# Performance work log

Hardware: AMD Instinct MI355X
Metric: run time of the kernel (lower is better)

## Reference

```python
import jax, jax.numpy as jnp
import numpy as np

GLYPH_DIM = 4096
PADDING_IDX = GLYPH_DIM  # 4096
GLYPH_EMB = 20           # CHAR_EMB 16 + COLOR_EMB 4
HIDDEN = 32
MAX_LEN = 64


def setup_inputs() -> dict:
    key = jax.random.key(0)
    k1, k2, k3, k4, k5, k6, k7 = jax.random.split(key, 7)
    B, H, W = 8192, 21, 79
    glyph_chars = jax.random.randint(k1, (B, H, W), 0, 256, dtype=jnp.int32)
    glyph_colors = jax.random.randint(k2, (B, H, W), 0, 16, dtype=jnp.int32)
    # Embedding table with zero padding row (torch padding_idx semantics)
    emb_table = jax.random.normal(k3, (GLYPH_DIM + 1, GLYPH_EMB), dtype=jnp.float32) * 0.02
    emb_table = emb_table.at[PADDING_IDX].set(0.0)
    s = 1.0 / np.sqrt(HIDDEN)
    W_ih = jax.random.uniform(k4, (HIDDEN, GLYPH_EMB), minval=-s, maxval=s, dtype=jnp.float32)
    W_hh = jax.random.uniform(k5, (HIDDEN, HIDDEN), minval=-s, maxval=s, dtype=jnp.float32)
    b_ih = jax.random.uniform(k6, (HIDDEN,), minval=-s, maxval=s, dtype=jnp.float32)
    b_hh = jax.random.uniform(k7, (HIDDEN,), minval=-s, maxval=s, dtype=jnp.float32)
    return {"glyph_chars": glyph_chars, "glyph_colors": glyph_colors,
            "emb_table": emb_table, "W_ih": W_ih, "W_hh": W_hh,
            "b_ih": b_ih, "b_hh": b_hh}


def _encode_bag(glyph_chars, glyph_colors):
    """Batched sorted-unique compaction over the bounded glyph id range."""
    B = glyph_chars.shape[0]
    g_ids = ((glyph_chars << 4) + glyph_colors).reshape(B, -1)  # [B, H*W]
    # presence[b, g] = glyph g appears in sample b (batched histogram)
    bidx = jnp.broadcast_to(jnp.arange(B, dtype=g_ids.dtype)[:, None], g_ids.shape)
    presence = jnp.zeros((B, GLYPH_DIM), dtype=bool).at[bidx, g_ids].set(True)
    # compact: present ids keep their value, absent become PADDING_IDX (=4096),
    # so sorting yields ascending unique ids followed by padding.
    ids = jnp.arange(GLYPH_DIM, dtype=jnp.int32)
    keys = jnp.where(presence, ids, jnp.int32(PADDING_IDX))
    bag = jnp.sort(keys, axis=1)[:, :MAX_LEN]  # [B, MAX_LEN]
    lengths = jnp.minimum(presence.sum(axis=1), MAX_LEN)  # [B]
    return bag, lengths


def reference(glyph_chars, glyph_colors, emb_table, W_ih, W_hh, b_ih, b_hh):
    bag, lengths = _encode_bag(glyph_chars, glyph_colors)
    emb = emb_table[bag]  # [B, MAX_LEN, GLYPH_EMB]
    B = emb.shape[0]

    # packed RNN == plain RNN where hidden state freezes past each sequence length
    xs = jnp.swapaxes(emb, 0, 1)  # [T, B, E]

    def step(h, inp):
        xt, t = inp
        h_new = jnp.tanh(xt @ W_ih.T + b_ih + h @ W_hh.T + b_hh)
        h = jnp.where((t < lengths)[:, None], h_new, h)
        return h, None

    h0 = jnp.zeros((B, HIDDEN), dtype=emb.dtype)
    h, _ = jax.lax.scan(step, h0, (xs, jnp.arange(MAX_LEN)))
    return (h, emb, bag)
```

## Files before the change

### kernel.cpp

```cpp
#include <hip/hip_runtime.h>

#define HW 1659
#define PADID 4096
#define EMB 20
#define HID 32
#define MAXLEN 64

__global__ __launch_bounds__(128) void proj_kernel(
    const float* __restrict__ emb_table, const float* __restrict__ W_ih,
    float* __restrict__ proj)
{
    const int tid = threadIdx.x;
    const int g = blockIdx.x * 4 + (tid >> 5);
    const int j = tid & 31;
    if (g > PADID) return;
    const float* er = emb_table + (size_t)g * EMB;
    const float* wr = W_ih + j * EMB;
    float s = 0.f;
#pragma unroll
    for (int k = 0; k < EMB; k++) s += wr[k] * er[k];
    proj[(size_t)g * HID + j] = s;
}

__global__ __launch_bounds__(256) void bag_emb_kernel(
    const int* __restrict__ chars, const int* __restrict__ colors,
    const float* __restrict__ emb_table,
    float* __restrict__ out_emb, float* __restrict__ out_bag)
{
    __shared__ unsigned char pres[4096];
    __shared__ int bagl[64];
    __shared__ int wsum[4];

    const int b   = blockIdx.x;
    const int tid = threadIdx.x;
    const int lane = tid & 63;
    const int wv   = tid >> 6;

    ((uint4*)pres)[tid] = make_uint4(0u, 0u, 0u, 0u);
    if (tid < 64) bagl[tid] = PADID;
    __syncthreads();

    const int base = b * HW;
    const int pe = (4 - (base & 3)) & 3;
    if (tid < pe) {
        int g = (chars[base + tid] << 4) + colors[base + tid];
        pres[g] = 1;
    }
    const int nv = (HW - pe) >> 2;
    const int nt = HW - pe - (nv << 2);
    const int4* c4 = (const int4*)(chars + base + pe);
    const int4* k4 = (const int4*)(colors + base + pe);
    for (int v = tid; v < nv; v += 256) {
        int4 c = c4[v], k = k4[v];
        pres[(c.x << 4) + k.x] = 1;
        pres[(c.y << 4) + k.y] = 1;
        pres[(c.z << 4) + k.z] = 1;
        pres[(c.w << 4) + k.w] = 1;
    }
    if (tid < nt) {
        int i = base + pe + (nv << 2) + tid;
        pres[(chars[i] << 4) + colors[i]] = 1;
    }
    __syncthreads();

    uint4 w4 = ((const uint4*)pres)[tid];
    const unsigned M = 0x01010101u;
    int cnt = __popc(w4.x & M) + __popc(w4.y & M)
            + __popc(w4.z & M) + __popc(w4.w & M);

    int pre = cnt;
#pragma unroll
    for (int d = 1; d < 64; d <<= 1) {
        int v = __shfl_up(pre, d, 64);
        if (lane >= d) pre += v;
    }
    if (lane == 63) wsum[wv] = pre;
    __syncthreads();
    int wbase = 0;
#pragma unroll
    for (int w2 = 0; w2 < 4; w2++) wbase += (w2 < wv) ? wsum[w2] : 0;
    int p = wbase + pre - cnt;

    unsigned wrd[4] = {w4.x, w4.y, w4.z, w4.w};
#pragma unroll
    for (int c = 0; c < 4; c++) {
#pragma unroll
        for (int k = 0; k < 4; k++) {
            if ((wrd[c] >> (8 * k)) & 1) {
                if (p < 64) bagl[p] = 16 * tid + 4 * c + k;
                p++;
            }
        }
    }
    __syncthreads();

    if (tid < 64) out_bag[(size_t)b * 64 + tid] = (float)bagl[tid];

    const float4* tab4 = (const float4*)emb_table;
    float4* dst4 = (float4*)(out_emb + (size_t)b * (MAXLEN * EMB));
    for (int q = tid; q < MAXLEN * 5; q += 256) {
        int t = q / 5;
        int m = q - t * 5;
        int row = bagl[t];
        dst4[q] = tab4[row * 5 + m];
    }
}

__global__ __launch_bounds__(128, 4) void rnn_kernel(
    const float* __restrict__ proj, const float* __restrict__ bagf,
    const float* __restrict__ W_hh,
    const float* __restrict__ b_ih, const float* __restrict__ b_hh,
    float* __restrict__ out_h)
{
    __shared__ float hbuf[8][32];

    const int tid  = threadIdx.x;
    const int wv   = tid >> 6;
    const int lane = tid & 63;
    const int sl   = lane >> 4;
    const int ib   = wv * 4 + sl;
    const int jj   = lane & 15;
    const int b    = blockIdx.x * 8 + ib;

    float w0[HID], w1[HID];
#pragma unroll
    for (int k = 0; k < HID; k++) {
        const int src = ((k & 1) << 4) + (k >> 1);
        w0[k] = W_hh[jj * HID + src];
        w1[k] = W_hh[(jj + 16) * HID + src];
    }
    const float sb0 = b_ih[jj] + b_hh[jj];
    const float sb1 = b_ih[jj + 16] + b_hh[jj + 16];

    const float* bps = bagf + (size_t)b * 64;

    unsigned long long mm0 = __ballot(bps[jj]      < 4095.5f);
    unsigned long long mm1 = __ballot(bps[jj + 16] < 4095.5f);
    unsigned long long mm2 = __ballot(bps[jj + 32] < 4095.5f);
    unsigned long long mm3 = __ballot(bps[jj + 48] < 4095.5f);
    const int sh = sl * 16;
    const int len = __popc((unsigned)((mm0 >> sh) & 0xFFFFu))
                  + __popc((unsigned)((mm1 >> sh) & 0xFFFFu))
                  + __popc((unsigned)((mm2 >> sh) & 0xFFFFu))
                  + __popc((unsigned)((mm3 >> sh) & 0xFFFFu));

    ((float2*)hbuf[ib])[jj] = make_float2(0.f, 0.f);
    asm volatile("s_waitcnt lgkmcnt(0)" ::: "memory");

    float h0 = 0.f, h1 = 0.f;
    for (int t = 0; t < MAXLEN; t++) {
        const int idx = (int)bps[t];
        const float pv0 = proj[idx * HID + jj];
        const float pv1 = proj[idx * HID + jj + 16];

        const float4* hb4 = (const float4*)hbuf[ib];
        float a0 = sb0 + pv0, a1 = sb1 + pv1, c0 = 0.f, c1 = 0.f;
#pragma unroll
        for (int m = 0; m < 8; m += 2) {
            float4 u = hb4[m], v = hb4[m + 1];
            a0 += w0[4*m+0]*u.x + w0[4*m+1]*u.y + w0[4*m+2]*u.z + w0[4*m+3]*u.w;
            a1 += w1[4*m+0]*u.x + w1[4*m+1]*u.y + w1[4*m+2]*u.z + w1[4*m+3]*u.w;
            c0 += w0[4*m+4]*v.x + w0[4*m+5]*v.y + w0[4*m+6]*v.z + w0[4*m+7]*v.w;
            c1 += w1[4*m+4]*v.x + w1[4*m+5]*v.y + w1[4*m+6]*v.z + w1[4*m+7]*v.w;
        }
        float s0 = a0 + c0, s1 = a1 + c1;

        s0 = fminf(fmaxf(s0, -9.f), 9.f);
        s1 = fminf(fmaxf(s1, -9.f), 9.f);
        float e0 = __expf(2.f * s0);
        float e1 = __expf(2.f * s1);
        float th0 = (e0 - 1.f) * __builtin_amdgcn_rcpf(e0 + 1.f);
        float th1 = (e1 - 1.f) * __builtin_amdgcn_rcpf(e1 + 1.f);

        h0 = (t < len) ? th0 : h0;
        h1 = (t < len) ? th1 : h1;

        ((float2*)hbuf[ib])[jj] = make_float2(h0, h1);
        asm volatile("s_waitcnt lgkmcnt(0)" ::: "memory");
    }

    out_h[(size_t)b * HID + jj]      = h0;
    out_h[(size_t)b * HID + jj + 16] = h1;
}

__global__ __launch_bounds__(128, 4) void rnn_kernel_noproj(
    const float* __restrict__ emb, const float* __restrict__ bagf,
    const float* __restrict__ W_ih, const float* __restrict__ W_hh,
    const float* __restrict__ b_ih, const float* __restrict__ b_hh,
    float* __restrict__ out_h)
{
    __shared__ float hbuf[4][32];
    const int tid = threadIdx.x;
    const int ib  = tid >> 5;
    const int j   = tid & 31;
    const int b   = blockIdx.x * 4 + ib;

    float wih[EMB];
#pragma unroll
    for (int k = 0; k < EMB; k++) wih[k] = W_ih[j * EMB + k];
    float whh[HID];
#pragma unroll
    for (int k = 0; k < HID; k++) whh[k] = W_hh[j * HID + k];
    const float sbias = b_ih[j] + b_hh[j];

    const float* bp = bagf + (size_t)b * 64;
    unsigned long long m0 = __ballot(bp[j]      < 4095.5f);
    unsigned long long m1 = __ballot(bp[32 + j] < 4095.5f);
    const int half = ib & 1;
    const int len = __popc((unsigned)(m0 >> (half * 32)))
                  + __popc((unsigned)(m1 >> (half * 32)));

    hbuf[ib][j] = 0.f;
    asm volatile("s_waitcnt lgkmcnt(0)" ::: "memory");

    float h = 0.f;
    const float* xb = emb + (size_t)b * (MAXLEN * EMB);
    for (int t = 0; t < MAXLEN; t++) {
        const float4* xp = (const float4*)(xb + t * EMB);
        float4 x0 = xp[0], x1 = xp[1], x2 = xp[2], x3 = xp[3], x4 = xp[4];
        float s = sbias;
        const float4* hb4 = (const float4*)hbuf[ib];
#pragma unroll
        for (int m = 0; m < 8; m++) {
            float4 hv = hb4[m];
            s += whh[4*m+0]*hv.x + whh[4*m+1]*hv.y
               + whh[4*m+2]*hv.z + whh[4*m+3]*hv.w;
        }
        s += wih[0]*x0.x + wih[1]*x0.y + wih[2]*x0.z + wih[3]*x0.w;
        s += wih[4]*x1.x + wih[5]*x1.y + wih[6]*x1.z + wih[7]*x1.w;
        s += wih[8]*x2.x + wih[9]*x2.y + wih[10]*x2.z + wih[11]*x2.w;
        s += wih[12]*x3.x + wih[13]*x3.y + wih[14]*x3.z + wih[15]*x3.w;
        s += wih[16]*x4.x + wih[17]*x4.y + wih[18]*x4.z + wih[19]*x4.w;
        s = fminf(fmaxf(s, -9.f), 9.f);
        float e = __expf(2.f * s);
        float th = (e - 1.f) * __builtin_amdgcn_rcpf(e + 1.f);
        h = (t < len) ? th : h;
        hbuf[ib][j] = h;
        asm volatile("s_waitcnt lgkmcnt(0)" ::: "memory");
    }
    out_h[(size_t)b * HID + j] = h;
}

extern "C" void kernel_launch(void* const* d_in, const int* in_sizes, int n_in,
                              void* d_out, int out_size, void* d_ws, size_t ws_size,
                              hipStream_t stream) {
    const int*   chars     = (const int*)d_in[0];
    const int*   colors    = (const int*)d_in[1];
    const float* emb_table = (const float*)d_in[2];
    const float* W_ih      = (const float*)d_in[3];
    const float* W_hh      = (const float*)d_in[4];
    const float* b_ih      = (const float*)d_in[5];
    const float* b_hh      = (const float*)d_in[6];

    const int B = in_sizes[0] / HW;

    float* out     = (float*)d_out;
    float* out_h   = out;
    float* out_emb = out + (size_t)B * HID;
    float* out_bag = out_emb + (size_t)B * MAXLEN * EMB;

    const size_t proj_bytes = (size_t)(PADID + 1) * HID * sizeof(float);

    bag_emb_kernel<<<B, 256, 0, stream>>>(chars, colors, emb_table, out_emb, out_bag);

    if (ws_size >= proj_bytes) {
        float* proj = (float*)d_ws;
        proj_kernel<<<(PADID + 1 + 3) / 4, 128, 0, stream>>>(emb_table, W_ih, proj);
        rnn_kernel<<<B / 8, 128, 0, stream>>>(proj, out_bag, W_hh, b_ih, b_hh, out_h);
    } else {
        rnn_kernel_noproj<<<B / 4, 128, 0, stream>>>(out_emb, out_bag, W_ih, W_hh,
                                                     b_ih, b_hh, out_h);
    }
}
```

Baseline: 194.5 us.

## Prefetch bag inputs before clear and pipeline RNN proj loads with packed FMA

In the bag kernel, the char/color vector loads are issued before the shared-memory clear and barrier, so global latency overlaps the initialization. In the RNN kernel, the projection row for the next step and the bag index two steps ahead are prefetched, which takes the dependent gather off the recurrent critical path. The W_hh dot products are rewritten as packed two-wide FMAs with a natural hidden-state layout, and tanh uses 1-2/(e+1) without the clamp. Removing the clamp relies on __expf overflowing to inf so that rcp yields 0; this adds register pressure and assumes nv <= 512.

```diff
diff --git a/kernel.cpp b/kernel.cpp
--- a/kernel.cpp
+++ b/kernel.cpp
@@ -5,6 +5,8 @@
 #define EMB 20
 #define HID 32
 #define MAXLEN 64
+
+typedef float v2f __attribute__((ext_vector_type(2)));
 
 __global__ __launch_bounds__(128) void proj_kernel(
     const float* __restrict__ emb_table, const float* __restrict__ W_ih,
@@ -36,31 +38,40 @@
     const int lane = tid & 63;
     const int wv   = tid >> 6;
 
-    ((uint4*)pres)[tid] = make_uint4(0u, 0u, 0u, 0u);
-    if (tid < 64) bagl[tid] = PADID;
-    __syncthreads();
-
     const int base = b * HW;
     const int pe = (4 - (base & 3)) & 3;
-    if (tid < pe) {
-        int g = (chars[base + tid] << 4) + colors[base + tid];
-        pres[g] = 1;
-    }
     const int nv = (HW - pe) >> 2;
     const int nt = HW - pe - (nv << 2);
     const int4* c4 = (const int4*)(chars + base + pe);
     const int4* k4 = (const int4*)(colors + base + pe);
-    for (int v = tid; v < nv; v += 256) {
-        int4 c = c4[v], k = k4[v];
-        pres[(c.x << 4) + k.x] = 1;
-        pres[(c.y << 4) + k.y] = 1;
-        pres[(c.z << 4) + k.z] = 1;
-        pres[(c.w << 4) + k.w] = 1;
-    }
+
+    int4 ca = c4[tid], ka = k4[tid];
+    const bool has2 = (tid + 256) < nv;
+    const int i2 = has2 ? tid + 256 : tid;
+    int4 cb = c4[i2], kb = k4[i2];
+    int gp = -1, gt = -1;
+    if (tid < pe) gp = (chars[base + tid] << 4) + colors[base + tid];
     if (tid < nt) {
         int i = base + pe + (nv << 2) + tid;
-        pres[(chars[i] << 4) + colors[i]] = 1;
-    }
+        gt = (chars[i] << 4) + colors[i];
+    }
+
+    ((uint4*)pres)[tid] = make_uint4(0u, 0u, 0u, 0u);
+    if (tid < 64) bagl[tid] = PADID;
+    __syncthreads();
+
+    pres[(ca.x << 4) + ka.x] = 1;
+    pres[(ca.y << 4) + ka.y] = 1;
+    pres[(ca.z << 4) + ka.z] = 1;
+    pres[(ca.w << 4) + ka.w] = 1;
+    if (has2) {
+        pres[(cb.x << 4) + kb.x] = 1;
+        pres[(cb.y << 4) + kb.y] = 1;
+        pres[(cb.z << 4) + kb.z] = 1;
+        pres[(cb.w << 4) + kb.w] = 1;
+    }
+    if (gp >= 0) pres[gp] = 1;
+    if (gt >= 0) pres[gt] = 1;
     __syncthreads();
 
     uint4 w4 = ((const uint4*)pres)[tid];
@@ -122,14 +133,13 @@
     const int jj   = lane & 15;
     const int b    = blockIdx.x * 8 + ib;
 
-    float w0[HID], w1[HID];
-#pragma unroll
-    for (int k = 0; k < HID; k++) {
-        const int src = ((k & 1) << 4) + (k >> 1);
-        w0[k] = W_hh[jj * HID + src];
-        w1[k] = W_hh[(jj + 16) * HID + src];
-    }
-    const float sb0 = b_ih[jj] + b_hh[jj];
+    v2f w0p[16], w1p[16];
+#pragma unroll
+    for (int m = 0; m < 16; m++) {
+        w0p[m] = (v2f){W_hh[jj * HID + 2*m], W_hh[jj * HID + 2*m + 1]};
+        w1p[m] = (v2f){W_hh[(jj+16) * HID + 2*m], W_hh[(jj+16) * HID + 2*m + 1]};
+    }
+    const float sb0 = b_ih[jj]      + b_hh[jj];
     const float sb1 = b_ih[jj + 16] + b_hh[jj + 16];
 
     const float* bps = bagf + (size_t)b * 64;
@@ -144,39 +154,56 @@
                   + __popc((unsigned)((mm2 >> sh) & 0xFFFFu))
                   + __popc((unsigned)((mm3 >> sh) & 0xFFFFu));
 
-    ((float2*)hbuf[ib])[jj] = make_float2(0.f, 0.f);
+    hbuf[ib][jj]      = 0.f;
+    hbuf[ib][jj + 16] = 0.f;
     asm volatile("s_waitcnt lgkmcnt(0)" ::: "memory");
+
+    int   idxB = (int)bps[0];
+    int   idxC = (int)bps[1];
+    float pv0 = proj[idxB * HID + jj];
+    float pv1 = proj[idxB * HID + jj + 16];
 
     float h0 = 0.f, h1 = 0.f;
     for (int t = 0; t < MAXLEN; t++) {
-        const int idx = (int)bps[t];
-        const float pv0 = proj[idx * HID + jj];
-        const float pv1 = proj[idx * HID + jj + 16];
+        const int t2 = (t + 2 < MAXLEN) ? (t + 2) : (MAXLEN - 1);
+        const int idxD = (int)bps[t2];
+        const float pv0n = proj[idxC * HID + jj];
+        const float pv1n = proj[idxC * HID + jj + 16];
 
         const float4* hb4 = (const float4*)hbuf[ib];
-        float a0 = sb0 + pv0, a1 = sb1 + pv1, c0 = 0.f, c1 = 0.f;
+        v2f a0 = (v2f){0.f, 0.f}, a1 = a0, c0 = a0, c1 = a0;
 #pragma unroll
         for (int m = 0; m < 8; m += 2) {
             float4 u = hb4[m], v = hb4[m + 1];
-            a0 += w0[4*m+0]*u.x + w0[4*m+1]*u.y + w0[4*m+2]*u.z + w0[4*m+3]*u.w;
-            a1 += w1[4*m+0]*u.x + w1[4*m+1]*u.y + w1[4*m+2]*u.z + w1[4*m+3]*u.w;
-            c0 += w0[4*m+4]*v.x + w0[4*m+5]*v.y + w0[4*m+6]*v.z + w0[4*m+7]*v.w;
-            c1 += w1[4*m+4]*v.x + w1[4*m+5]*v.y + w1[4*m+6]*v.z + w1[4*m+7]*v.w;
+            v2f ulo = (v2f){u.x, u.y}, uhi = (v2f){u.z, u.w};
+            v2f vlo = (v2f){v.x, v.y}, vhi = (v2f){v.z, v.w};
+            a0 = __builtin_elementwise_fma(w0p[2*m],     ulo, a0);
+            a0 = __builtin_elementwise_fma(w0p[2*m + 1], uhi, a0);
+            a1 = __builtin_elementwise_fma(w1p[2*m],     ulo, a1);
+            a1 = __builtin_elementwise_fma(w1p[2*m + 1], uhi, a1);
+            c0 = __builtin_elementwise_fma(w0p[2*m + 2], vlo, c0);
+            c0 = __builtin_elementwise_fma(w0p[2*m + 3], vhi, c0);
+            c1 = __builtin_elementwise_fma(w1p[2*m + 2], vlo, c1);
+            c1 = __builtin_elementwise_fma(w1p[2*m + 3], vhi, c1);
         }
-        float s0 = a0 + c0, s1 = a1 + c1;
-
-        s0 = fminf(fmaxf(s0, -9.f), 9.f);
-        s1 = fminf(fmaxf(s1, -9.f), 9.f);
+        v2f t0 = a0 + c0;
+        v2f t1 = a1 + c1;
+        float s0 = sb0 + pv0 + t0.x + t0.y;
+        float s1 = sb1 + pv1 + t1.x + t1.y;
+
         float e0 = __expf(2.f * s0);
         float e1 = __expf(2.f * s1);
-        float th0 = (e0 - 1.f) * __builtin_amdgcn_rcpf(e0 + 1.f);
-        float th1 = (e1 - 1.f) * __builtin_amdgcn_rcpf(e1 + 1.f);
+        float th0 = 1.f - 2.f * __builtin_amdgcn_rcpf(e0 + 1.f);
+        float th1 = 1.f - 2.f * __builtin_amdgcn_rcpf(e1 + 1.f);
 
         h0 = (t < len) ? th0 : h0;
         h1 = (t < len) ? th1 : h1;
 
-        ((float2*)hbuf[ib])[jj] = make_float2(h0, h1);
+        hbuf[ib][jj]      = h0;
+        hbuf[ib][jj + 16] = h1;
         asm volatile("s_waitcnt lgkmcnt(0)" ::: "memory");
+
+        pv0 = pv0n; pv1 = pv1n; idxC = idxD;
     }
 
     out_h[(size_t)b * HID + jj]      = h0;
```

Result: faster. 185.6 us (-4.6%).
